# Optimization experiments

Measured on AMD Instinct MI355X. Metric: run time of the kernel, lower is better.

Reference implementation:

```python
import jax, jax.numpy as jnp
import numpy as np

N_QUBITS = 4
N_LAYERS = 3
N_FEATURES = 64
BATCH = 524288


def setup_inputs() -> dict:
    key = jax.random.key(0)
    k1, k2, k3, k4 = jax.random.split(key, 4)
    x = jax.random.normal(k1, (BATCH, N_FEATURES), jnp.float32)
    # nn.Linear(64, 4) params
    lim = 1.0 / np.sqrt(N_FEATURES)
    W_pre = jax.random.uniform(k2, (N_QUBITS, N_FEATURES), jnp.float32, -lim, lim)
    b_pre = jax.random.uniform(k3, (N_QUBITS,), jnp.float32, -lim, lim)
    # quantum circuit weights: randn * 0.1
    qweights = jax.random.normal(k4, (N_LAYERS, N_QUBITS, 2), jnp.float32) * 0.1
    return {"x": x, "W_pre": W_pre, "b_pre": b_pre, "qweights": qweights}


def _coef(theta, n):
    # reshape scalar or [B] angle to broadcast against [B, 2,..,2] (n-1 trailing dims after slicing)
    return jnp.reshape(theta, (-1,) + (1,) * (n - 1))


def _apply_ry(state, wire, theta):
    # RY(t) = [[cos t/2, -sin t/2], [sin t/2, cos t/2]] applied on `wire`
    n = state.ndim - 1
    s = jnp.moveaxis(state, 1 + wire, -1)
    a, b = s[..., 0], s[..., 1]
    c = _coef(jnp.cos(theta / 2), n)
    sn = _coef(jnp.sin(theta / 2), n)
    out = jnp.stack([c * a - sn * b, sn * a + c * b], axis=-1)
    return jnp.moveaxis(out, -1, 1 + wire)


def _apply_rz(state, wire, theta):
    # RZ(t) = diag(e^{-i t/2}, e^{+i t/2})
    n = state.ndim - 1
    s = jnp.moveaxis(state, 1 + wire, -1)
    half = _coef(theta / 2, n)
    out = jnp.stack([jnp.exp(-1j * half) * s[..., 0],
                     jnp.exp(1j * half) * s[..., 1]], axis=-1)
    return jnp.moveaxis(out, -1, 1 + wire)


def _apply_cnot(state, ctrl, tgt):
    s = jnp.moveaxis(state, (1 + ctrl, 1 + tgt), (-2, -1))
    s = jnp.concatenate([s[..., 0:1, :], s[..., 1:2, ::-1]], axis=-2)
    return jnp.moveaxis(s, (-2, -1), (1 + ctrl, 1 + tgt))


def _circuit(angles, qweights):
    # batched 4-qubit statevector simulation; state shape [B, 2,2,2,2] (wire 0 = MSB)
    B, n = angles.shape
    nl = qweights.shape[0]
    state = jnp.zeros((B,) + (2,) * n, jnp.complex64)
    state = state.at[(slice(None),) + (0,) * n].set(1.0)
    for w in range(n):
        state = _apply_ry(state, w, angles[:, w])
    for l in range(nl):
        for w in range(n):
            state = _apply_ry(state, w, qweights[l, w, 0])
            state = _apply_rz(state, w, qweights[l, w, 1])
        for w in range(n):
            state = _apply_cnot(state, w, (w + 1) % n)
    probs = state.real ** 2 + state.imag ** 2  # [B, 2,2,2,2] float32
    exps = []
    for w in range(n):
        marg = jnp.moveaxis(probs, 1 + w, 1).reshape(B, 2, -1).sum(-1)  # [B, 2]
        exps.append(marg[:, 0] - marg[:, 1])  # <Z_w>
    return jnp.stack(exps, axis=1)  # [B, n]


def reference(x, W_pre, b_pre, qweights):
    angles = jnp.tanh(x @ W_pre.T + b_pre)  # [B, n_qubits]
    return _circuit(angles, qweights).astype(jnp.float32)
```

## Files before the change

kernel.cpp:

```cpp
#include <hip/hip_runtime.h>
#include <cmath>

__global__ __launch_bounds__(256) void qfused_kernel(
    const float* __restrict__ x,
    const float* __restrict__ Wp,
    const float* __restrict__ bp,
    const float* __restrict__ qw,
    float* __restrict__ out)
{
  __shared__ float lds[4352 + 324];
  constexpr int SRE = 0;
  constexpr int SIM = 272;
  constexpr int MOF = 544;
  constexpr int AOF = 4352;
  float* xt = lds;

  const int tid = threadIdx.x;
  const size_t row0 = (size_t)blockIdx.x * 256;

  float4 rbuf[4];
  {
    const int rrow = tid >> 2, q4 = (tid & 3) << 2;
#pragma unroll
    for (int p = 0; p < 4; ++p)
      rbuf[p] = *reinterpret_cast<const float4*>(
          x + (row0 + (size_t)(p * 64 + rrow)) * 64 + 0 * 16 + q4);
  }

  {
    const int col = tid >> 4;
    const int u   = tid & 15;
    lds[SRE + col * 17 + u] = (u == col) ? 1.0f : 0.0f;
    lds[SIM + col * 17 + u] = 0.0f;
    __syncthreads();

#pragma unroll
    for (int l = 0; l < 3; ++l) {
#pragma unroll
      for (int w = 0; w < 4; ++w) {
        const int mask = 8 >> w;
        float sh, ch, sh2, ch2;
        __sincosf(0.5f * qw[(l * 4 + w) * 2 + 0], &sh, &ch);
        __sincosf(0.5f * qw[(l * 4 + w) * 2 + 1], &sh2, &ch2);
        const int ua = u & ~mask, ub = u | mask;
        const float ar = lds[SRE + col * 17 + ua], ai = lds[SIM + col * 17 + ua];
        const float br = lds[SRE + col * 17 + ub], bi = lds[SIM + col * 17 + ub];
        __syncthreads();
        float nr, ni;
        if (u & mask) { nr = sh * ar + ch * br; ni = sh * ai + ch * bi; }
        else          { nr = ch * ar - sh * br; ni = ch * ai - sh * bi; }
        float rr, ri;
        if (u & mask) { rr = ch2 * nr - sh2 * ni; ri = ch2 * ni + sh2 * nr; }
        else          { rr = ch2 * nr + sh2 * ni; ri = ch2 * ni - sh2 * nr; }
        lds[SRE + col * 17 + u] = rr; lds[SIM + col * 17 + u] = ri;
        __syncthreads();
      }
      int src = u;
      if (src & 1) src ^= 8;
      if (src & 2) src ^= 1;
      if (src & 4) src ^= 2;
      if (src & 8) src ^= 4;
      const float pr = lds[SRE + col * 17 + src], pi = lds[SIM + col * 17 + src];
      __syncthreads();
      lds[SRE + col * 17 + u] = pr; lds[SIM + col * 17 + u] = pi;
      __syncthreads();
    }

#pragma unroll
    for (int k = 0; k < 4; ++k) {
      const int idx = tid + 256 * k;
      const int w = idx >> 8, s = (idx >> 4) & 15, t = idx & 15;
      const int mask = 8 >> w;
      float acc = 0.0f;
#pragma unroll
      for (int uu = 0; uu < 16; ++uu) {
        const float z = (uu & mask) ? -1.0f : 1.0f;
        acc += z * (lds[SRE + s * 17 + uu] * lds[SRE + t * 17 + uu] +
                    lds[SIM + s * 17 + uu] * lds[SIM + t * 17 + uu]);
      }
      lds[MOF + ((w * 16 + s) * 16 + t)] = acc;
    }
    __syncthreads();

    for (int idx = tid; idx < 324; idx += 256) {
      const int w = idx & 3, pq = idx >> 2;
      const int p = pq / 9, q = pq % 9;
      const int i0 = p / 3, i1 = p % 3, i2 = q / 3, i3 = q % 3;
      float acc = 0.0f;
#pragma unroll
      for (int comb = 0; comb < 16; ++comb) {
        int s = 0, t = 0;
        float coef = 0.0625f;
        int j;
        j = (comb >> 3) & 1; s |= j << 3; t |= ((i0 == 2) ? (j ^ 1) : j) << 3; if (i0 == 1 && j) coef = -coef;
        j = (comb >> 2) & 1; s |= j << 2; t |= ((i1 == 2) ? (j ^ 1) : j) << 2; if (i1 == 1 && j) coef = -coef;
        j = (comb >> 1) & 1; s |= j << 1; t |= ((i2 == 2) ? (j ^ 1) : j) << 1; if (i2 == 1 && j) coef = -coef;
        j = comb & 1;        s |= j;      t |= ((i3 == 2) ? (j ^ 1) : j);      if (i3 == 1 && j) coef = -coef;
        acc = fmaf(coef, lds[MOF + ((w * 16 + s) * 16 + t)], acc);
      }
      lds[AOF + idx] = acc;
    }
    __syncthreads();
  }

  const int rrow = tid >> 2, q4 = (tid & 3) << 2;
  float a0 = 0.f, a1 = 0.f, a2 = 0.f, a3 = 0.f;
#pragma unroll
  for (int c = 0; c < 4; ++c) {
#pragma unroll
    for (int p = 0; p < 4; ++p) {
      float* d = &xt[(p * 64 + rrow) * 17 + q4];
      d[0] = rbuf[p].x; d[1] = rbuf[p].y; d[2] = rbuf[p].z; d[3] = rbuf[p].w;
    }
    if (c < 3) {
#pragma unroll
      for (int p = 0; p < 4; ++p)
        rbuf[p] = *reinterpret_cast<const float4*>(
            x + (row0 + (size_t)(p * 64 + rrow)) * 64 + (c + 1) * 16 + q4);
    }
    __syncthreads();
#pragma unroll
    for (int f = 0; f < 16; ++f) {
      const float xv = xt[tid * 17 + f];
      const int fg = c * 16 + f;
      a0 = fmaf(xv, Wp[fg], a0);
      a1 = fmaf(xv, Wp[64 + fg], a1);
      a2 = fmaf(xv, Wp[128 + fg], a2);
      a3 = fmaf(xv, Wp[192 + fg], a3);
    }
    if (c < 3) __syncthreads();
  }

  const float t0 = 1.0f - 2.0f / (__expf(2.0f * (a0 + bp[0])) + 1.0f);
  const float t1 = 1.0f - 2.0f / (__expf(2.0f * (a1 + bp[1])) + 1.0f);
  const float t2 = 1.0f - 2.0f / (__expf(2.0f * (a2 + bp[2])) + 1.0f);
  const float t3 = 1.0f - 2.0f / (__expf(2.0f * (a3 + bp[3])) + 1.0f);

  float c0, s0, c1, s1, c2, s2, c3, s3;
  __sincosf(t0, &s0, &c0);
  __sincosf(t1, &s1, &c1);
  __sincosf(t2, &s2, &c2);
  __sincosf(t3, &s3, &c3);

  const float g[9] = {1.f, c1, s1, c0, c0 * c1, c0 * s1, s0, s0 * c1, s0 * s1};
  const float h[9] = {1.f, c3, s3, c2, c2 * c3, c2 * s3, s2, s2 * c3, s2 * s3};

  float e0 = 0.f, e1 = 0.f, e2 = 0.f, e3 = 0.f;
#pragma unroll
  for (int p = 0; p < 9; ++p) {
#pragma unroll
    for (int q = 0; q < 9; ++q) {
      const float t = g[p] * h[q];
      const int base = AOF + (p * 9 + q) * 4;
      e0 = fmaf(lds[base + 0], t, e0);
      e1 = fmaf(lds[base + 1], t, e1);
      e2 = fmaf(lds[base + 2], t, e2);
      e3 = fmaf(lds[base + 3], t, e3);
    }
  }
  reinterpret_cast<float4*>(out)[row0 + tid] = make_float4(e0, e1, e2, e3);
}

extern "C" void kernel_launch(void* const* d_in, const int* in_sizes, int n_in,
                              void* d_out, int out_size, void* d_ws, size_t ws_size,
                              hipStream_t stream) {
  const float* x  = (const float*)d_in[0];
  const float* Wp = (const float*)d_in[1];
  const float* bp = (const float*)d_in[2];
  const float* qw = (const float*)d_in[3];
  float* out = (float*)d_out;

  const int B = in_sizes[0] / 64;
  qfused_kernel<<<B / 256, 256, 0, stream>>>(x, Wp, bp, qw, out);
}
```

Measured before the change: 41.70 us.

## Process two 256-row tiles per block to amortize per-block circuit setup

Each block now handles 512 rows instead of 256, so the circuit-matrix precomputation in LDS (the many-barrier unitary build and the 324-coefficient reduction) is paid once per 512 rows instead of once per 256. The x load becomes a double-buffered register prefetch across eight 16-feature chunks, LDS staging uses float4 stores and loads with a padded stride of 20, and the final contraction reads the coefficients as float4 and shares each load between both rows. It adds launch_bounds occupancy 4. The cost is higher register pressure and half as many blocks, which may reduce latency hiding.

Measured after the change: 77.06 us. 1.85x slower.

```diff
diff --git a/kernel.cpp b/kernel.cpp
--- a/kernel.cpp
+++ b/kernel.cpp
@@ -1,31 +1,60 @@
 #include <hip/hip_runtime.h>
 #include <cmath>
 
-__global__ __launch_bounds__(256) void qfused_kernel(
+
+#define XADDR(R, P) \
+  (x + (row0 + (size_t)((((R) >> 2) * 256) + (P) * 64 + rrow)) * 64 + \
+   (size_t)((((R) & 3) * 16) + q4))
+
+#define PREFETCH(RB, R)                                      \
+  RB[0] = *reinterpret_cast<const float4*>(XADDR(R, 0));     \
+  RB[1] = *reinterpret_cast<const float4*>(XADDR(R, 1));     \
+  RB[2] = *reinterpret_cast<const float4*>(XADDR(R, 2));     \
+  RB[3] = *reinterpret_cast<const float4*>(XADDR(R, 3));
+
+#define STAGE_WRITE(RB)                                                       \
+  *reinterpret_cast<float4*>(&lds[(0 * 64 + rrow) * XS + q4]) = RB[0];        \
+  *reinterpret_cast<float4*>(&lds[(1 * 64 + rrow) * XS + q4]) = RB[1];        \
+  *reinterpret_cast<float4*>(&lds[(2 * 64 + rrow) * XS + q4]) = RB[2];        \
+  *reinterpret_cast<float4*>(&lds[(3 * 64 + rrow) * XS + q4]) = RB[3];
+
+#define GEMV(A0, A1, A2, A3, C) {                                             \
+  const float4 xv0 = *reinterpret_cast<const float4*>(&lds[tid * XS + 0]);    \
+  const float4 xv1 = *reinterpret_cast<const float4*>(&lds[tid * XS + 4]);    \
+  const float4 xv2 = *reinterpret_cast<const float4*>(&lds[tid * XS + 8]);    \
+  const float4 xv3 = *reinterpret_cast<const float4*>(&lds[tid * XS + 12]);   \
+  const float xr[16] = {xv0.x, xv0.y, xv0.z, xv0.w, xv1.x, xv1.y, xv1.z,      \
+                        xv1.w, xv2.x, xv2.y, xv2.z, xv2.w, xv3.x, xv3.y,      \
+                        xv3.z, xv3.w};                                        \
+  _Pragma("unroll")                                                           \
+  for (int f = 0; f < 16; ++f) {                                              \
+    A0 = fmaf(xr[f], Wp[(C) * 16 + f], A0);                                   \
+    A1 = fmaf(xr[f], Wp[64 + (C) * 16 + f], A1);                              \
+    A2 = fmaf(xr[f], Wp[128 + (C) * 16 + f], A2);                             \
+    A3 = fmaf(xr[f], Wp[192 + (C) * 16 + f], A3);                             \
+  } }
+
+__global__ __launch_bounds__(256, 4) void qfused_kernel(
     const float* __restrict__ x,
     const float* __restrict__ Wp,
     const float* __restrict__ bp,
     const float* __restrict__ qw,
     float* __restrict__ out)
 {
-  __shared__ float lds[4352 + 324];
+  constexpr int XS  = 20;
+  constexpr int AOF = 256 * XS;
+  __shared__ alignas(16) float lds[256 * XS + 324];
   constexpr int SRE = 0;
   constexpr int SIM = 272;
   constexpr int MOF = 544;
-  constexpr int AOF = 4352;
-  float* xt = lds;
 
   const int tid = threadIdx.x;
-  const size_t row0 = (size_t)blockIdx.x * 256;
-
-  float4 rbuf[4];
-  {
-    const int rrow = tid >> 2, q4 = (tid & 3) << 2;
-#pragma unroll
-    for (int p = 0; p < 4; ++p)
-      rbuf[p] = *reinterpret_cast<const float4*>(
-          x + (row0 + (size_t)(p * 64 + rrow)) * 64 + 0 * 16 + q4);
-  }
+  const size_t row0 = (size_t)blockIdx.x * 512;
+  const int rrow = tid >> 2, q4 = (tid & 3) << 2;
+
+  float4 rbA[4], rbB[4];
+  PREFETCH(rbA, 0);
+  PREFETCH(rbB, 1);
 
   {
     const int col = tid >> 4;
@@ -103,62 +132,76 @@
     __syncthreads();
   }
 
-  const int rrow = tid >> 2, q4 = (tid & 3) << 2;
-  float a0 = 0.f, a1 = 0.f, a2 = 0.f, a3 = 0.f;
-#pragma unroll
-  for (int c = 0; c < 4; ++c) {
-#pragma unroll
-    for (int p = 0; p < 4; ++p) {
-      float* d = &xt[(p * 64 + rrow) * 17 + q4];
-      d[0] = rbuf[p].x; d[1] = rbuf[p].y; d[2] = rbuf[p].z; d[3] = rbuf[p].w;
-    }
-    if (c < 3) {
-#pragma unroll
-      for (int p = 0; p < 4; ++p)
-        rbuf[p] = *reinterpret_cast<const float4*>(
-            x + (row0 + (size_t)(p * 64 + rrow)) * 64 + (c + 1) * 16 + q4);
-    }
-    __syncthreads();
-#pragma unroll
-    for (int f = 0; f < 16; ++f) {
-      const float xv = xt[tid * 17 + f];
-      const int fg = c * 16 + f;
-      a0 = fmaf(xv, Wp[fg], a0);
-      a1 = fmaf(xv, Wp[64 + fg], a1);
-      a2 = fmaf(xv, Wp[128 + fg], a2);
-      a3 = fmaf(xv, Wp[192 + fg], a3);
-    }
-    if (c < 3) __syncthreads();
-  }
-
-  const float t0 = 1.0f - 2.0f / (__expf(2.0f * (a0 + bp[0])) + 1.0f);
-  const float t1 = 1.0f - 2.0f / (__expf(2.0f * (a1 + bp[1])) + 1.0f);
-  const float t2 = 1.0f - 2.0f / (__expf(2.0f * (a2 + bp[2])) + 1.0f);
-  const float t3 = 1.0f - 2.0f / (__expf(2.0f * (a3 + bp[3])) + 1.0f);
-
-  float c0, s0, c1, s1, c2, s2, c3, s3;
-  __sincosf(t0, &s0, &c0);
-  __sincosf(t1, &s1, &c1);
-  __sincosf(t2, &s2, &c2);
-  __sincosf(t3, &s3, &c3);
-
-  const float g[9] = {1.f, c1, s1, c0, c0 * c1, c0 * s1, s0, s0 * c1, s0 * s1};
-  const float h[9] = {1.f, c3, s3, c2, c2 * c3, c2 * s3, s2, s2 * c3, s2 * s3};
-
-  float e0 = 0.f, e1 = 0.f, e2 = 0.f, e3 = 0.f;
+  float aA0 = 0.f, aA1 = 0.f, aA2 = 0.f, aA3 = 0.f;
+  float aB0 = 0.f, aB1 = 0.f, aB2 = 0.f, aB3 = 0.f;
+
+  STAGE_WRITE(rbA); PREFETCH(rbA, 2); __syncthreads();
+  GEMV(aA0, aA1, aA2, aA3, 0); __syncthreads();
+  STAGE_WRITE(rbB); PREFETCH(rbB, 3); __syncthreads();
+  GEMV(aA0, aA1, aA2, aA3, 1); __syncthreads();
+  STAGE_WRITE(rbA); PREFETCH(rbA, 4); __syncthreads();
+  GEMV(aA0, aA1, aA2, aA3, 2); __syncthreads();
+  STAGE_WRITE(rbB); PREFETCH(rbB, 5); __syncthreads();
+  GEMV(aA0, aA1, aA2, aA3, 3); __syncthreads();
+
+  float g0[9], h0[9];
+  {
+    const float t0 = 1.0f - 2.0f / (__expf(2.0f * (aA0 + bp[0])) + 1.0f);
+    const float t1 = 1.0f - 2.0f / (__expf(2.0f * (aA1 + bp[1])) + 1.0f);
+    const float t2 = 1.0f - 2.0f / (__expf(2.0f * (aA2 + bp[2])) + 1.0f);
+    const float t3 = 1.0f - 2.0f / (__expf(2.0f * (aA3 + bp[3])) + 1.0f);
+    float c0, s0, c1, s1, c2, s2, c3, s3;
+    __sincosf(t0, &s0, &c0); __sincosf(t1, &s1, &c1);
+    __sincosf(t2, &s2, &c2); __sincosf(t3, &s3, &c3);
+    g0[0] = 1.f; g0[1] = c1; g0[2] = s1; g0[3] = c0; g0[4] = c0 * c1;
+    g0[5] = c0 * s1; g0[6] = s0; g0[7] = s0 * c1; g0[8] = s0 * s1;
+    h0[0] = 1.f; h0[1] = c3; h0[2] = s3; h0[3] = c2; h0[4] = c2 * c3;
+    h0[5] = c2 * s3; h0[6] = s2; h0[7] = s2 * c3; h0[8] = s2 * s3;
+  }
+
+  STAGE_WRITE(rbA); PREFETCH(rbA, 6); __syncthreads();
+  GEMV(aB0, aB1, aB2, aB3, 0); __syncthreads();
+  STAGE_WRITE(rbB); PREFETCH(rbB, 7); __syncthreads();
+  GEMV(aB0, aB1, aB2, aB3, 1); __syncthreads();
+  STAGE_WRITE(rbA); __syncthreads();
+  GEMV(aB0, aB1, aB2, aB3, 2); __syncthreads();
+  STAGE_WRITE(rbB); __syncthreads();
+  GEMV(aB0, aB1, aB2, aB3, 3);
+
+  float g1[9], h1[9];
+  {
+    const float t0 = 1.0f - 2.0f / (__expf(2.0f * (aB0 + bp[0])) + 1.0f);
+    const float t1 = 1.0f - 2.0f / (__expf(2.0f * (aB1 + bp[1])) + 1.0f);
+    const float t2 = 1.0f - 2.0f / (__expf(2.0f * (aB2 + bp[2])) + 1.0f);
+    const float t3 = 1.0f - 2.0f / (__expf(2.0f * (aB3 + bp[3])) + 1.0f);
+    float c0, s0, c1, s1, c2, s2, c3, s3;
+    __sincosf(t0, &s0, &c0); __sincosf(t1, &s1, &c1);
+    __sincosf(t2, &s2, &c2); __sincosf(t3, &s3, &c3);
+    g1[0] = 1.f; g1[1] = c1; g1[2] = s1; g1[3] = c0; g1[4] = c0 * c1;
+    g1[5] = c0 * s1; g1[6] = s0; g1[7] = s0 * c1; g1[8] = s0 * s1;
+    h1[0] = 1.f; h1[1] = c3; h1[2] = s3; h1[3] = c2; h1[4] = c2 * c3;
+    h1[5] = c2 * s3; h1[6] = s2; h1[7] = s2 * c3; h1[8] = s2 * s3;
+  }
+
+  float e00 = 0.f, e01 = 0.f, e02 = 0.f, e03 = 0.f;
+  float e10 = 0.f, e11 = 0.f, e12 = 0.f, e13 = 0.f;
 #pragma unroll
   for (int p = 0; p < 9; ++p) {
 #pragma unroll
     for (int q = 0; q < 9; ++q) {
-      const float t = g[p] * h[q];
-      const int base = AOF + (p * 9 + q) * 4;
-      e0 = fmaf(lds[base + 0], t, e0);
-      e1 = fmaf(lds[base + 1], t, e1);
-      e2 = fmaf(lds[base + 2], t, e2);
-      e3 = fmaf(lds[base + 3], t, e3);
-    }
-  }
-  reinterpret_cast<float4*>(out)[row0 + tid] = make_float4(e0, e1, e2, e3);
+      const float4 a4 =
+          *reinterpret_cast<const float4*>(&lds[AOF + (p * 9 + q) * 4]);
+      const float tA = g0[p] * h0[q];
+      const float tB = g1[p] * h1[q];
+      e00 = fmaf(a4.x, tA, e00); e01 = fmaf(a4.y, tA, e01);
+      e02 = fmaf(a4.z, tA, e02); e03 = fmaf(a4.w, tA, e03);
+      e10 = fmaf(a4.x, tB, e10); e11 = fmaf(a4.y, tB, e11);
+      e12 = fmaf(a4.z, tB, e12); e13 = fmaf(a4.w, tB, e13);
+    }
+  }
+  float4* out4 = reinterpret_cast<float4*>(out);
+  out4[row0 + tid]       = make_float4(e00, e01, e02, e03);
+  out4[row0 + 256 + tid] = make_float4(e10, e11, e12, e13);
 }
 
 extern "C" void kernel_launch(void* const* d_in, const int* in_sizes, int n_in,
@@ -169,7 +212,8 @@
   const float* bp = (const float*)d_in[2];
   const float* qw = (const float*)d_in[3];
   float* out = (float*)d_out;
+  (void)d_ws; (void)ws_size;
 
   const int B = in_sizes[0] / 64;
-  qfused_kernel<<<B / 256, 256, 0, stream>>>(x, Wp, bp, qw, out);
+  qfused_kernel<<<B / 512, 256, 0, stream>>>(x, Wp, bp, qw, out);
 }
```

## Compute linear projection with wave shuffles instead of LDS transpose

Applied to the files above, without the earlier changes.

Replaces the LDS-staged transpose of x, in which each thread computed one row's dot product, with a scheme where 16 lanes each take a float4 slice of a row, compute partial dot products with W held in registers, and reduce them with xor shuffles. The x loads are software-pipelined four float4s deep, the LDS footprint shrinks, the coefficient table is read as float4, and a waves_per_eu attribute is added. This removes the per-chunk LDS stores, reads and barriers, but adds 16 shuffles per row group and wasted redundant lanes during the reduction.

Result: slower. 48.49 us (+16.3%).

```diff
diff --git a/kernel.cpp b/kernel.cpp
--- a/kernel.cpp
+++ b/kernel.cpp
@@ -1,31 +1,32 @@
 #include <hip/hip_runtime.h>
 #include <cmath>
 
-__global__ __launch_bounds__(256) void qfused_kernel(
+
+__global__ __launch_bounds__(256)
+__attribute__((amdgpu_waves_per_eu(4, 4)))
+void qfused_kernel(
     const float* __restrict__ x,
     const float* __restrict__ Wp,
     const float* __restrict__ bp,
     const float* __restrict__ qw,
     float* __restrict__ out)
 {
-  __shared__ float lds[4352 + 324];
-  constexpr int SRE = 0;
-  constexpr int SIM = 272;
-  constexpr int MOF = 544;
-  constexpr int AOF = 4352;
-  float* xt = lds;
+  constexpr int AOF = 0;
+  constexpr int SRE = 328;
+  constexpr int SIM = 600;
+  constexpr int MOF = 872;
+  __shared__ alignas(16) float lds[872 + 1024];
 
-  const int tid = threadIdx.x;
-  const size_t row0 = (size_t)blockIdx.x * 256;
+  const int tid  = threadIdx.x;
+  const int lane = tid & 63;
+  const int q    = lane >> 4;
+  const int f4   = lane & 15;
 
-  float4 rbuf[4];
-  {
-    const int rrow = tid >> 2, q4 = (tid & 3) << 2;
-#pragma unroll
-    for (int p = 0; p < 4; ++p)
-      rbuf[p] = *reinterpret_cast<const float4*>(
-          x + (row0 + (size_t)(p * 64 + rrow)) * 64 + 0 * 16 + q4);
-  }
+  const size_t base = ((size_t)blockIdx.x * 4 + (tid >> 6)) * 64;
+  const float4* xw = reinterpret_cast<const float4*>(x) +
+                     base * 16 + (size_t)q * 16 + f4;
+
+  float4 p0 = xw[0], p1 = xw[64], p2 = xw[128], p3 = xw[192];
 
   {
     const int col = tid >> 4;
@@ -84,8 +85,8 @@
 
     for (int idx = tid; idx < 324; idx += 256) {
       const int w = idx & 3, pq = idx >> 2;
-      const int p = pq / 9, q = pq % 9;
-      const int i0 = p / 3, i1 = p % 3, i2 = q / 3, i3 = q % 3;
+      const int p = pq / 9, qq = pq % 9;
+      const int i0 = p / 3, i1 = p % 3, i2 = qq / 3, i3 = qq % 3;
       float acc = 0.0f;
 #pragma unroll
       for (int comb = 0; comb < 16; ++comb) {
@@ -103,44 +104,60 @@
     __syncthreads();
   }
 
-  const int rrow = tid >> 2, q4 = (tid & 3) << 2;
-  float a0 = 0.f, a1 = 0.f, a2 = 0.f, a3 = 0.f;
-#pragma unroll
-  for (int c = 0; c < 4; ++c) {
-#pragma unroll
-    for (int p = 0; p < 4; ++p) {
-      float* d = &xt[(p * 64 + rrow) * 17 + q4];
-      d[0] = rbuf[p].x; d[1] = rbuf[p].y; d[2] = rbuf[p].z; d[3] = rbuf[p].w;
-    }
-    if (c < 3) {
-#pragma unroll
-      for (int p = 0; p < 4; ++p)
-        rbuf[p] = *reinterpret_cast<const float4*>(
-            x + (row0 + (size_t)(p * 64 + rrow)) * 64 + (c + 1) * 16 + q4);
-    }
-    __syncthreads();
-#pragma unroll
-    for (int f = 0; f < 16; ++f) {
-      const float xv = xt[tid * 17 + f];
-      const int fg = c * 16 + f;
-      a0 = fmaf(xv, Wp[fg], a0);
-      a1 = fmaf(xv, Wp[64 + fg], a1);
-      a2 = fmaf(xv, Wp[128 + fg], a2);
-      a3 = fmaf(xv, Wp[192 + fg], a3);
-    }
-    if (c < 3) __syncthreads();
+  const float4* W4 = reinterpret_cast<const float4*>(Wp);
+  const float4 w0 = W4[0 * 16 + f4];
+  const float4 w1 = W4[1 * 16 + f4];
+  const float4 w2 = W4[2 * 16 + f4];
+  const float4 w3 = W4[3 * 16 + f4];
+
+  float sa0 = 0.f, sa1 = 0.f, sa2 = 0.f, sa3 = 0.f;
+
+#define COMP(i, PV) {                                                        \
+    float r0 = fmaf(PV.x, w0.x, fmaf(PV.y, w0.y,                             \
+               fmaf(PV.z, w0.z, PV.w * w0.w)));                              \
+    float r1 = fmaf(PV.x, w1.x, fmaf(PV.y, w1.y,                             \
+               fmaf(PV.z, w1.z, PV.w * w1.w)));                              \
+    float r2 = fmaf(PV.x, w2.x, fmaf(PV.y, w2.y,                             \
+               fmaf(PV.z, w2.z, PV.w * w2.w)));                              \
+    float r3 = fmaf(PV.x, w3.x, fmaf(PV.y, w3.y,                             \
+               fmaf(PV.z, w3.z, PV.w * w3.w)));                              \
+    r0 += __shfl_xor(r0, 1, 64); r0 += __shfl_xor(r0, 2, 64);                \
+    r0 += __shfl_xor(r0, 4, 64); r0 += __shfl_xor(r0, 8, 64);                \
+    r1 += __shfl_xor(r1, 1, 64); r1 += __shfl_xor(r1, 2, 64);                \
+    r1 += __shfl_xor(r1, 4, 64); r1 += __shfl_xor(r1, 8, 64);                \
+    r2 += __shfl_xor(r2, 1, 64); r2 += __shfl_xor(r2, 2, 64);                \
+    r2 += __shfl_xor(r2, 4, 64); r2 += __shfl_xor(r2, 8, 64);                \
+    r3 += __shfl_xor(r3, 1, 64); r3 += __shfl_xor(r3, 2, 64);                \
+    r3 += __shfl_xor(r3, 4, 64); r3 += __shfl_xor(r3, 8, 64);                \
+    if (f4 == (i)) { sa0 = r0; sa1 = r1; sa2 = r2; sa3 = r3; }               \
   }
 
-  const float t0 = 1.0f - 2.0f / (__expf(2.0f * (a0 + bp[0])) + 1.0f);
-  const float t1 = 1.0f - 2.0f / (__expf(2.0f * (a1 + bp[1])) + 1.0f);
-  const float t2 = 1.0f - 2.0f / (__expf(2.0f * (a2 + bp[2])) + 1.0f);
-  const float t3 = 1.0f - 2.0f / (__expf(2.0f * (a3 + bp[3])) + 1.0f);
+  COMP(0, p0);  p0 = xw[64 * 4];
+  COMP(1, p1);  p1 = xw[64 * 5];
+  COMP(2, p2);  p2 = xw[64 * 6];
+  COMP(3, p3);  p3 = xw[64 * 7];
+  COMP(4, p0);  p0 = xw[64 * 8];
+  COMP(5, p1);  p1 = xw[64 * 9];
+  COMP(6, p2);  p2 = xw[64 * 10];
+  COMP(7, p3);  p3 = xw[64 * 11];
+  COMP(8, p0);  p0 = xw[64 * 12];
+  COMP(9, p1);  p1 = xw[64 * 13];
+  COMP(10, p2); p2 = xw[64 * 14];
+  COMP(11, p3); p3 = xw[64 * 15];
+  COMP(12, p0);
+  COMP(13, p1);
+  COMP(14, p2);
+  COMP(15, p3);
+#undef COMP
+
+  const float t0 = 1.0f - 2.0f / (__expf(2.0f * (sa0 + bp[0])) + 1.0f);
+  const float t1 = 1.0f - 2.0f / (__expf(2.0f * (sa1 + bp[1])) + 1.0f);
+  const float t2 = 1.0f - 2.0f / (__expf(2.0f * (sa2 + bp[2])) + 1.0f);
+  const float t3 = 1.0f - 2.0f / (__expf(2.0f * (sa3 + bp[3])) + 1.0f);
 
   float c0, s0, c1, s1, c2, s2, c3, s3;
-  __sincosf(t0, &s0, &c0);
-  __sincosf(t1, &s1, &c1);
-  __sincosf(t2, &s2, &c2);
-  __sincosf(t3, &s3, &c3);
+  __sincosf(t0, &s0, &c0); __sincosf(t1, &s1, &c1);
+  __sincosf(t2, &s2, &c2); __sincosf(t3, &s3, &c3);
 
   const float g[9] = {1.f, c1, s1, c0, c0 * c1, c0 * s1, s0, s0 * c1, s0 * s1};
   const float h[9] = {1.f, c3, s3, c2, c2 * c3, c2 * s3, s2, s2 * c3, s2 * s3};
@@ -149,16 +166,16 @@
 #pragma unroll
   for (int p = 0; p < 9; ++p) {
 #pragma unroll
-    for (int q = 0; q < 9; ++q) {
-      const float t = g[p] * h[q];
-      const int base = AOF + (p * 9 + q) * 4;
-      e0 = fmaf(lds[base + 0], t, e0);
-      e1 = fmaf(lds[base + 1], t, e1);
-      e2 = fmaf(lds[base + 2], t, e2);
-      e3 = fmaf(lds[base + 3], t, e3);
+    for (int qq = 0; qq < 9; ++qq) {
+      const float4 a4 =
+          *reinterpret_cast<const float4*>(&lds[AOF + (p * 9 + qq) * 4]);
+      const float t = g[p] * h[qq];
+      e0 = fmaf(a4.x, t, e0); e1 = fmaf(a4.y, t, e1);
+      e2 = fmaf(a4.z, t, e2); e3 = fmaf(a4.w, t, e3);
     }
   }
-  reinterpret_cast<float4*>(out)[row0 + tid] = make_float4(e0, e1, e2, e3);
+  reinterpret_cast<float4*>(out)[base + 4 * f4 + q] =
+      make_float4(e0, e1, e2, e3);
 }
 
 extern "C" void kernel_launch(void* const* d_in, const int* in_sizes, int n_in,
@@ -169,6 +186,7 @@
   const float* bp = (const float*)d_in[2];
   const float* qw = (const float*)d_in[3];
   float* out = (float*)d_out;
+  (void)d_ws; (void)ws_size; (void)n_in; (void)out_size;
 
   const int B = in_sizes[0] / 64;
   qfused_kernel<<<B / 256, 256, 0, stream>>>(x, Wp, bp, qw, out);
```
